# Performance work log

Measured on AMD Instinct MI355X. Metric: run time of the kernel, lower is better.

The kernel has to match this reference:

```python
import jax, jax.numpy as jnp
import numpy as np

DIM = 512
HEADS = 8
HEAD_DIM = DIM // HEADS

def setup_inputs() -> dict:
    key = jax.random.key(0)
    ks = jax.random.split(key, 5)
    s = 1.0 / np.sqrt(DIM)
    x = jax.random.normal(ks[0], (4, 2048, DIM), dtype=jnp.float32)
    w_qkv = jax.random.uniform(ks[1], (DIM, 3 * DIM), jnp.float32, -s, s)
    b_qkv = jax.random.uniform(ks[2], (3 * DIM,), jnp.float32, -s, s)
    w_out = jax.random.uniform(ks[3], (DIM, DIM), jnp.float32, -s, s)
    b_out = jax.random.uniform(ks[4], (DIM,), jnp.float32, -s, s)
    return {"x": x, "w_qkv": w_qkv, "b_qkv": b_qkv, "w_out": w_out, "b_out": b_out}

def reference(x, w_qkv, b_qkv, w_out, b_out):
    B, N, D = x.shape
    qkv = x @ w_qkv + b_qkv  # [B, N, 3D]
    qkv = qkv.reshape(B, N, 3, HEADS, HEAD_DIM).transpose(2, 0, 3, 1, 4)  # [3, B, H, N, hd]
    q, k, v = qkv[0], qkv[1], qkv[2]
    scale = 1.0 / np.sqrt(HEAD_DIM).astype(np.float32)
    attn = jnp.einsum('bhqd,bhkd->bhqk', q, k) * scale
    attn = jax.nn.softmax(attn, axis=-1)
    out = jnp.einsum('bhqk,bhkd->bhqd', attn, v)  # [B, H, N, hd]
    out = out.transpose(0, 2, 1, 3).reshape(B, N, D)
    return out @ w_out + b_out
```

## Files before the change

### kernel.cpp

```cpp
#include <hip/hip_runtime.h>

#define NB 4
#define NH 8
#define HD 64
#define DIMV 512
#define NSEQ 2048
#define QKVLD 1536
#define NTOK (NB*NSEQ)
#define KVB 64
#define QSCALE 0.18033688011112042f

typedef __attribute__((ext_vector_type(8))) short s8v;
typedef __attribute__((ext_vector_type(4))) float f4v;

typedef __attribute__((address_space(1))) void gvoid;
typedef __attribute__((address_space(3))) void lvoid;

__device__ __forceinline__ void load_lds16(const void* g, void* l){
  __builtin_amdgcn_global_load_lds((gvoid*)(void*)g, (lvoid*)l, 16, 0, 0);
}

__device__ __forceinline__ ushort f2bf(float f){
  unsigned u = __float_as_uint(f);
  u += 0x7fffu + ((u >> 16) & 1u);
  return (ushort)(u >> 16);
}

__device__ __forceinline__ unsigned pk2bf(float a, float b){
  return (unsigned)f2bf(a) | ((unsigned)f2bf(b) << 16);
}

__device__ __forceinline__ unsigned cvt_pk_bf16(float lo, float hi){
  unsigned r;
  asm("v_cvt_pk_bf16_f32 %0, %1, %2" : "=v"(r) : "v"(lo), "v"(hi));
  return r;
}
__device__ __forceinline__ float fexp2(float x){
  float r;
  asm("v_exp_f32 %0, %1" : "=v"(r) : "v"(x));
  return r;
}
__device__ __forceinline__ void plane32(unsigned &a, unsigned &b){
  asm("v_permlane32_swap_b32 %0, %1" : "+v"(a), "+v"(b));
}
__device__ __forceinline__ void plane16(unsigned &a, unsigned &b){
  asm("v_permlane16_swap_b32 %0, %1" : "+v"(a), "+v"(b));
}

__global__ __launch_bounds__(256) void k_prep(const float* __restrict__ x,
                                              ushort* __restrict__ xb,
                                              const float* __restrict__ w_qkv,
                                              ushort* __restrict__ wqkvT,
                                              const float* __restrict__ w_out,
                                              ushort* __restrict__ woutT){
  const int blk = blockIdx.x;
  const int tid = threadIdx.x;
  if (blk < 4096){
    const int i = blk * 256 + tid;
    float4 v = ((const float4*)x)[i];
    ushort4 o;
    o.x = f2bf(v.x); o.y = f2bf(v.y); o.z = f2bf(v.z); o.w = f2bf(v.w);
    ((ushort4*)xb)[i] = o;
    return;
  }
  __shared__ float t[32][33];
  const float* in; ushort* out; int C, bx, by;
  if (blk < 4864){
    const int idx = blk - 4096;
    in = w_qkv; out = wqkvT; C = QKVLD;
    bx = (idx % 48) * 32; by = (idx / 48) * 32;
  } else {
    const int idx = blk - 4864;
    in = w_out; out = woutT; C = DIMV;
    bx = (idx & 15) * 32; by = (idx >> 4) * 32;
  }
  const int tx = tid & 31, ty = tid >> 5;
  #pragma unroll
  for (int j = 0; j < 32; j += 8)
    t[ty + j][tx] = in[(size_t)(by + ty + j)*C + bx + tx];
  __syncthreads();
  #pragma unroll
  for (int j = 0; j < 32; j += 8)
    out[(size_t)(bx + ty + j)*DIMV + by + tx] = f2bf(t[tx][ty + j]);
}

template<bool SWAP>
__device__ __forceinline__ void gemm_kloop(const ushort* __restrict__ A,
                                           const ushort* __restrict__ Bt,
                                           ushort* As, ushort* Bs,
                                           int tm, int tn, int K,
                                           int w, int l, int lr, int lg,
                                           f4v acc[4][4]){
  const int r8 = l >> 3;
  const int lc = (l & 7) ^ r8;
  const int swz = (lr & 7) << 4;
  for (int kk = 0; kk < K; kk += 64){
    __syncthreads();
    #pragma unroll
    for (int c = 0; c < 4; ++c){
      const int ci = w*4 + c;
      const int row = ci*8 + r8;
      load_lds16(A  + (size_t)(tm + row)*K + kk + lc*8, (char*)As + ci*1024);
      load_lds16(Bt + (size_t)(tn + row)*K + kk + lc*8, (char*)Bs + ci*1024);
    }
    __syncthreads();
    const int wm = (w >> 1), wn = (w & 1);
    s8v af[4][2], bf[4][2];
    #pragma unroll
    for (int i = 0; i < 4; ++i){
      const int ra = (wm*64 + i*16 + lr)*128;
      const int rb = (wn*64 + i*16 + lr)*128;
      #pragma unroll
      for (int t = 0; t < 2; ++t){
        af[i][t] = *(const s8v*)((const char*)As + ra + ((t*64 + lg*16) ^ swz));
        bf[i][t] = *(const s8v*)((const char*)Bs + rb + ((t*64 + lg*16) ^ swz));
      }
    }
    #pragma unroll
    for (int mi = 0; mi < 4; ++mi)
      #pragma unroll
      for (int ni = 0; ni < 4; ++ni){
        if (SWAP){
          acc[mi][ni] = __builtin_amdgcn_mfma_f32_16x16x32_bf16(bf[ni][0], af[mi][0], acc[mi][ni], 0, 0, 0);
          acc[mi][ni] = __builtin_amdgcn_mfma_f32_16x16x32_bf16(bf[ni][1], af[mi][1], acc[mi][ni], 0, 0, 0);
        } else {
          acc[mi][ni] = __builtin_amdgcn_mfma_f32_16x16x32_bf16(af[mi][0], bf[ni][0], acc[mi][ni], 0, 0, 0);
          acc[mi][ni] = __builtin_amdgcn_mfma_f32_16x16x32_bf16(af[mi][1], bf[ni][1], acc[mi][ni], 0, 0, 0);
        }
      }
  }
}

template<int MODE, int NCT>
__global__ __launch_bounds__(256) void k_gemm(const ushort* __restrict__ A,
                                              const ushort* __restrict__ Bt,
                                              const float* __restrict__ bias,
                                              void* __restrict__ Cout,
                                              ushort* __restrict__ vtp,
                                              int N, int K){
  __shared__ ushort As[128*64];
  __shared__ ushort Bs[128*64];
  const int tid = threadIdx.x;
  const int w = tid >> 6, l = tid & 63;
  const int lr = l & 15, lg = l >> 4;
  const int wm = w >> 1, wn = w & 1;
  const int wg = blockIdx.x;
  const int xcd = wg & 7, idx = wg >> 3;
  const int tn = (idx % NCT) * 128;
  const int tm = (xcd * 8 + idx / NCT) * 128;
  f4v acc[4][4] = {};

  if (MODE == 0 && tn >= 2*DIMV){
    gemm_kloop<false>(A, Bt, As, Bs, tm, tn, K, w, l, lr, lg, acc);
    const int b = tm >> 11;
    const int n0 = (tm & (NSEQ-1)) + wm*64;
    #pragma unroll
    for (int ni = 0; ni < 4; ++ni){
      const int c = tn + wn*64 + ni*16 + lr;
      const int hd_i = c - 2*DIMV;
      const float bv = bias[c];
      ushort* vrow = vtp + ((size_t)(b*DIMV + hd_i))*NSEQ;
      #pragma unroll
      for (int mi = 0; mi < 4; ++mi){
        const int n = n0 + mi*16 + lg*4;
        uint2 pk;
        pk.x = pk2bf(acc[mi][ni][0] + bv, acc[mi][ni][1] + bv);
        pk.y = pk2bf(acc[mi][ni][2] + bv, acc[mi][ni][3] + bv);
        *(uint2*)(vrow + n) = pk;
      }
    }
    return;
  }

  gemm_kloop<true>(A, Bt, As, Bs, tm, tn, K, w, l, lr, lg, acc);

  if (MODE == 0){
    ushort* C = (ushort*)Cout;
    const float sc = (tn < DIMV) ? QSCALE : 1.0f;
    #pragma unroll
    for (int ni = 0; ni < 4; ++ni){
      const int c0 = tn + wn*64 + ni*16 + lg*4;
      const float4 bv = *(const float4*)(bias + c0);
      #pragma unroll
      for (int mi = 0; mi < 4; ++mi){
        const int r = tm + wm*64 + mi*16 + lr;
        uint2 pk;
        pk.x = pk2bf((acc[mi][ni][0] + bv.x)*sc, (acc[mi][ni][1] + bv.y)*sc);
        pk.y = pk2bf((acc[mi][ni][2] + bv.z)*sc, (acc[mi][ni][3] + bv.w)*sc);
        *(uint2*)(C + (size_t)r*N + c0) = pk;
      }
    }
  } else {
    float* C = (float*)Cout;
    #pragma unroll
    for (int ni = 0; ni < 4; ++ni){
      const int c0 = tn + wn*64 + ni*16 + lg*4;
      const float4 bv = *(const float4*)(bias + c0);
      #pragma unroll
      for (int mi = 0; mi < 4; ++mi){
        const int r = tm + wm*64 + mi*16 + lr;
        float4 st;
        st.x = acc[mi][ni][0] + bv.x;
        st.y = acc[mi][ni][1] + bv.y;
        st.z = acc[mi][ni][2] + bv.z;
        st.w = acc[mi][ni][3] + bv.w;
        *(float4*)(C + (size_t)r*N + c0) = st;
      }
    }
  }
}

__global__ __launch_bounds__(256, 2) void k_attn(const ushort* __restrict__ qkv,
                                                 const ushort* __restrict__ vt,
                                                 ushort* __restrict__ ao){
  __shared__ alignas(1024) char smem[2][16384];
  const int tid = threadIdx.x;
  const int w = tid >> 6, l = tid & 63;
  const int lr = l & 15, lg = l >> 4;
  const int wg = blockIdx.x;
  const int n = (wg & 7) * 64 + (wg >> 3);
  const int bh = n >> 4, xt = n & 15;
  const int b = bh >> 3, h = bh & 7;
  const int q0 = xt * 128 + w * 32;

  const ushort* qpA = qkv + (size_t)(b*NSEQ + q0 + lr)*QKVLD + h*HD + lg*8;
  const ushort* qpB = qpA + (size_t)16*QKVLD;
  const s8v qfA0 = *(const s8v*)(qpA);
  const s8v qfA1 = *(const s8v*)(qpA + 32);
  const s8v qfB0 = *(const s8v*)(qpB);
  const s8v qfB1 = *(const s8v*)(qpB + 32);

  const int r8 = l >> 3;
  const int lc = (l & 7) ^ r8;
  const int wbase = w * 16;
  const ushort* kg0 = qkv + (size_t)(b*NSEQ + wbase + r8)*QKVLD + DIMV + h*HD + lc*8;
  const ushort* kg1 = kg0 + (size_t)8*QKVLD;
  const ushort* vg0 = vt + (size_t)(bh*HD + wbase + r8)*NSEQ + lc*8;
  const ushort* vg1 = vg0 + (size_t)8*NSEQ;

  float lsumA = 0.0f, lsumB = 0.0f;
  f4v oA[4] = {}, oB[4] = {};

  load_lds16(kg0, &smem[0][ wbase   *128]);
  load_lds16(kg1, &smem[0][(wbase+8)*128]);
  load_lds16(vg0, &smem[0][ wbase   *128 + 8192]);
  load_lds16(vg1, &smem[0][(wbase+8)*128 + 8192]);
  kg0 += (size_t)KVB*QKVLD; kg1 += (size_t)KVB*QKVLD; vg0 += KVB; vg1 += KVB;

  const int swz = (lr & 7) << 4;
  const int ro0 = lr*128 + ((     lg*16) ^ swz);
  const int ro1 = lr*128 + ((64 + lg*16) ^ swz);

  for (int kt = 0; kt < NSEQ/KVB; ++kt){
    const int cur = kt & 1;
    __syncthreads();

    if (kt + 1 < NSEQ/KVB){
      char* dst = &smem[cur^1][0];
      load_lds16(kg0, dst +  wbase   *128);
      load_lds16(kg1, dst + (wbase+8)*128);
      load_lds16(vg0, dst +  wbase   *128 + 8192);
      load_lds16(vg1, dst + (wbase+8)*128 + 8192);
      kg0 += (size_t)KVB*QKVLD; kg1 += (size_t)KVB*QKVLD; vg0 += KVB; vg1 += KVB;
    }

    const char* b0 = &smem[cur][0] + ro0;
    const char* b1 = &smem[cur][0] + ro1;

    f4v sA[4] = {}, sB[4] = {};
    __builtin_amdgcn_s_setprio(1);
    #pragma unroll
    for (int kb = 0; kb < 4; ++kb){
      const s8v kf0 = *(const s8v*)(b0 + kb*2048);
      const s8v kf1 = *(const s8v*)(b1 + kb*2048);
      sA[kb] = __builtin_amdgcn_mfma_f32_16x16x32_bf16(kf0, qfA0, sA[kb], 0,0,0);
      sA[kb] = __builtin_amdgcn_mfma_f32_16x16x32_bf16(kf1, qfA1, sA[kb], 0,0,0);
      sB[kb] = __builtin_amdgcn_mfma_f32_16x16x32_bf16(kf0, qfB0, sB[kb], 0,0,0);
      sB[kb] = __builtin_amdgcn_mfma_f32_16x16x32_bf16(kf1, qfB1, sB[kb], 0,0,0);
    }
    __builtin_amdgcn_s_setprio(0);

    union { uint4 u; s8v v; } pfA0, pfA1, pfB0, pfB1;
    {
      const float p0 = fexp2(sA[0][0]), p1 = fexp2(sA[0][1]);
      const float p2 = fexp2(sA[0][2]), p3 = fexp2(sA[0][3]);
      const float p4 = fexp2(sA[1][0]), p5 = fexp2(sA[1][1]);
      const float p6 = fexp2(sA[1][2]), p7 = fexp2(sA[1][3]);
      lsumA += ((p0 + p1) + (p2 + p3)) + ((p4 + p5) + (p6 + p7));
      unsigned a = cvt_pk_bf16(p0, p1), bq = cvt_pk_bf16(p4, p5);
      plane32(a, bq); plane16(a, bq);
      unsigned c = cvt_pk_bf16(p2, p3), d = cvt_pk_bf16(p6, p7);
      plane32(c, d);  plane16(c, d);
      pfA0.u.x = a; pfA0.u.y = c; pfA0.u.z = bq; pfA0.u.w = d;
    }
    {
      const float p0 = fexp2(sA[2][0]), p1 = fexp2(sA[2][1]);
      const float p2 = fexp2(sA[2][2]), p3 = fexp2(sA[2][3]);
      const float p4 = fexp2(sA[3][0]), p5 = fexp2(sA[3][1]);
      const float p6 = fexp2(sA[3][2]), p7 = fexp2(sA[3][3]);
      lsumA += ((p0 + p1) + (p2 + p3)) + ((p4 + p5) + (p6 + p7));
      unsigned a = cvt_pk_bf16(p0, p1), bq = cvt_pk_bf16(p4, p5);
      plane32(a, bq); plane16(a, bq);
      unsigned c = cvt_pk_bf16(p2, p3), d = cvt_pk_bf16(p6, p7);
      plane32(c, d);  plane16(c, d);
      pfA1.u.x = a; pfA1.u.y = c; pfA1.u.z = bq; pfA1.u.w = d;
    }
    {
      const float p0 = fexp2(sB[0][0]), p1 = fexp2(sB[0][1]);
      const float p2 = fexp2(sB[0][2]), p3 = fexp2(sB[0][3]);
      const float p4 = fexp2(sB[1][0]), p5 = fexp2(sB[1][1]);
      const float p6 = fexp2(sB[1][2]), p7 = fexp2(sB[1][3]);
      lsumB += ((p0 + p1) + (p2 + p3)) + ((p4 + p5) + (p6 + p7));
      unsigned a = cvt_pk_bf16(p0, p1), bq = cvt_pk_bf16(p4, p5);
      plane32(a, bq); plane16(a, bq);
      unsigned c = cvt_pk_bf16(p2, p3), d = cvt_pk_bf16(p6, p7);
      plane32(c, d);  plane16(c, d);
      pfB0.u.x = a; pfB0.u.y = c; pfB0.u.z = bq; pfB0.u.w = d;
    }
    {
      const float p0 = fexp2(sB[2][0]), p1 = fexp2(sB[2][1]);
      const float p2 = fexp2(sB[2][2]), p3 = fexp2(sB[2][3]);
      const float p4 = fexp2(sB[3][0]), p5 = fexp2(sB[3][1]);
      const float p6 = fexp2(sB[3][2]), p7 = fexp2(sB[3][3]);
      lsumB += ((p0 + p1) + (p2 + p3)) + ((p4 + p5) + (p6 + p7));
      unsigned a = cvt_pk_bf16(p0, p1), bq = cvt_pk_bf16(p4, p5);
      plane32(a, bq); plane16(a, bq);
      unsigned c = cvt_pk_bf16(p2, p3), d = cvt_pk_bf16(p6, p7);
      plane32(c, d);  plane16(c, d);
      pfB1.u.x = a; pfB1.u.y = c; pfB1.u.z = bq; pfB1.u.w = d;
    }

    __builtin_amdgcn_s_setprio(1);
    #pragma unroll
    for (int ni = 0; ni < 4; ++ni){
      const s8v vf0 = *(const s8v*)(b0 + 8192 + ni*2048);
      const s8v vf1 = *(const s8v*)(b1 + 8192 + ni*2048);
      oA[ni] = __builtin_amdgcn_mfma_f32_16x16x32_bf16(vf0, pfA0.v, oA[ni], 0,0,0);
      oA[ni] = __builtin_amdgcn_mfma_f32_16x16x32_bf16(vf1, pfA1.v, oA[ni], 0,0,0);
      oB[ni] = __builtin_amdgcn_mfma_f32_16x16x32_bf16(vf0, pfB0.v, oB[ni], 0,0,0);
      oB[ni] = __builtin_amdgcn_mfma_f32_16x16x32_bf16(vf1, pfB1.v, oB[ni], 0,0,0);
    }
    __builtin_amdgcn_s_setprio(0);
  }

  float ltA = lsumA;
  ltA += __shfl_xor(ltA, 16, 64);
  ltA += __shfl_xor(ltA, 32, 64);
  float ltB = lsumB;
  ltB += __shfl_xor(ltB, 16, 64);
  ltB += __shfl_xor(ltB, 32, 64);
  const float invA = 1.0f / ltA;
  const float invB = 1.0f / ltB;
  ushort* opA = ao + (size_t)(b*NSEQ + q0 + lr)*DIMV + h*HD;
  ushort* opB = opA + (size_t)16*DIMV;
  #pragma unroll
  for (int ni = 0; ni < 4; ++ni){
    uint2 pk;
    pk.x = cvt_pk_bf16(oA[ni][0]*invA, oA[ni][1]*invA);
    pk.y = cvt_pk_bf16(oA[ni][2]*invA, oA[ni][3]*invA);
    *(uint2*)(opA + ni*16 + lg*4) = pk;
    pk.x = cvt_pk_bf16(oB[ni][0]*invB, oB[ni][1]*invB);
    pk.y = cvt_pk_bf16(oB[ni][2]*invB, oB[ni][3]*invB);
    *(uint2*)(opB + ni*16 + lg*4) = pk;
  }
}


extern "C" void kernel_launch(void* const* d_in, const int* in_sizes, int n_in,
                              void* d_out, int out_size, void* d_ws, size_t ws_size,
                              hipStream_t stream) {
  (void)in_sizes; (void)n_in; (void)out_size; (void)ws_size;
  const float* x     = (const float*)d_in[0];
  const float* w_qkv = (const float*)d_in[1];
  const float* b_qkv = (const float*)d_in[2];
  const float* w_out = (const float*)d_in[3];
  const float* b_out = (const float*)d_in[4];
  float* out = (float*)d_out;

  char* ws = (char*)d_ws;
  ushort* xb    = (ushort*)(ws);
  ushort* wqkvT = (ushort*)(ws + 8388608);
  ushort* woutT = (ushort*)(ws + 8388608 + 1572864);
  ushort* qkv   = (ushort*)(ws + 10485760);
  ushort* vt    = (ushort*)(ws + 35651584);
  ushort* ao    = (ushort*)(ws + 44040192);

  k_prep<<<dim3(4096 + 768 + 256), 256, 0, stream>>>(x, xb, w_qkv, wqkvT, w_out, woutT);
  k_gemm<0,12><<<dim3(768), 256, 0, stream>>>(xb, wqkvT, b_qkv, qkv, vt, QKVLD, DIMV);
  k_attn<<<dim3(512), 256, 0, stream>>>(qkv, vt, ao);
  k_gemm<1,4><<<dim3(256), 256, 0, stream>>>(ao, woutT, b_out, out, nullptr, DIMV, DIMV);
}
```

Measured before the change: 90.20 us.

## Fuse x fp32-to-bf16 conversion into QKV GEMM and compute softmax row sums via MFMA

Drops the separate conversion pass that wrote a bf16 copy of x. The QKV GEMM now loads fp32 x directly, converts it in registers and stores it into LDS, saving a 16 MB read plus an 8 MB write and round trip. The cost is that each x tile is re-converted by all 12 column tiles, and the A-operand path becomes synchronous register loads instead of async global-to-LDS. Separately, the attention kernel computes softmax denominators with an extra MFMA against a ones vector, removing scalar adds and cross-lane shuffles at the price of four more MFMAs per KV block and sums taken over bf16-rounded probabilities.

```diff
diff --git a/kernel.cpp b/kernel.cpp
--- a/kernel.cpp
+++ b/kernel.cpp
@@ -47,30 +47,19 @@
   asm("v_permlane16_swap_b32 %0, %1" : "+v"(a), "+v"(b));
 }
 
-__global__ __launch_bounds__(256) void k_prep(const float* __restrict__ x,
-                                              ushort* __restrict__ xb,
-                                              const float* __restrict__ w_qkv,
+__global__ __launch_bounds__(256) void k_prep(const float* __restrict__ w_qkv,
                                               ushort* __restrict__ wqkvT,
                                               const float* __restrict__ w_out,
                                               ushort* __restrict__ woutT){
   const int blk = blockIdx.x;
   const int tid = threadIdx.x;
-  if (blk < 4096){
-    const int i = blk * 256 + tid;
-    float4 v = ((const float4*)x)[i];
-    ushort4 o;
-    o.x = f2bf(v.x); o.y = f2bf(v.y); o.z = f2bf(v.z); o.w = f2bf(v.w);
-    ((ushort4*)xb)[i] = o;
-    return;
-  }
   __shared__ float t[32][33];
   const float* in; ushort* out; int C, bx, by;
-  if (blk < 4864){
-    const int idx = blk - 4096;
+  if (blk < 768){
     in = w_qkv; out = wqkvT; C = QKVLD;
-    bx = (idx % 48) * 32; by = (idx / 48) * 32;
+    bx = (blk % 48) * 32; by = (blk / 48) * 32;
   } else {
-    const int idx = blk - 4864;
+    const int idx = blk - 768;
     in = w_out; out = woutT; C = DIMV;
     bx = (idx & 15) * 32; by = (idx >> 4) * 32;
   }
@@ -84,8 +73,8 @@
     out[(size_t)(bx + ty + j)*DIMV + by + tx] = f2bf(t[tx][ty + j]);
 }
 
-template<bool SWAP>
-__device__ __forceinline__ void gemm_kloop(const ushort* __restrict__ A,
+template<bool SWAP, bool CONV>
+__device__ __forceinline__ void gemm_kloop(const void* __restrict__ Asrc,
                                            const ushort* __restrict__ Bt,
                                            ushort* As, ushort* Bs,
                                            int tm, int tn, int K,
@@ -100,7 +89,20 @@
     for (int c = 0; c < 4; ++c){
       const int ci = w*4 + c;
       const int row = ci*8 + r8;
-      load_lds16(A  + (size_t)(tm + row)*K + kk + lc*8, (char*)As + ci*1024);
+      if (CONV){
+        const float* xs = (const float*)Asrc + (size_t)(tm + row)*K + kk + lc*8;
+        const float4 a0 = *(const float4*)(xs);
+        const float4 a1 = *(const float4*)(xs + 4);
+        uint4 wb;
+        wb.x = cvt_pk_bf16(a0.x, a0.y);
+        wb.y = cvt_pk_bf16(a0.z, a0.w);
+        wb.z = cvt_pk_bf16(a1.x, a1.y);
+        wb.w = cvt_pk_bf16(a1.z, a1.w);
+        *(uint4*)((char*)As + ci*1024 + l*16) = wb;
+      } else {
+        load_lds16((const ushort*)Asrc + (size_t)(tm + row)*K + kk + lc*8,
+                   (char*)As + ci*1024);
+      }
       load_lds16(Bt + (size_t)(tn + row)*K + kk + lc*8, (char*)Bs + ci*1024);
     }
     __syncthreads();
@@ -132,7 +134,7 @@
 }
 
 template<int MODE, int NCT>
-__global__ __launch_bounds__(256) void k_gemm(const ushort* __restrict__ A,
+__global__ __launch_bounds__(256) void k_gemm(const void* __restrict__ A,
                                               const ushort* __restrict__ Bt,
                                               const float* __restrict__ bias,
                                               void* __restrict__ Cout,
@@ -151,7 +153,7 @@
   f4v acc[4][4] = {};
 
   if (MODE == 0 && tn >= 2*DIMV){
-    gemm_kloop<false>(A, Bt, As, Bs, tm, tn, K, w, l, lr, lg, acc);
+    gemm_kloop<false, true>(A, Bt, As, Bs, tm, tn, K, w, l, lr, lg, acc);
     const int b = tm >> 11;
     const int n0 = (tm & (NSEQ-1)) + wm*64;
     #pragma unroll
@@ -172,7 +174,8 @@
     return;
   }
 
-  gemm_kloop<true>(A, Bt, As, Bs, tm, tn, K, w, l, lr, lg, acc);
+  if (MODE == 0) gemm_kloop<true, true >(A, Bt, As, Bs, tm, tn, K, w, l, lr, lg, acc);
+  else           gemm_kloop<true, false>(A, Bt, As, Bs, tm, tn, K, w, l, lr, lg, acc);
 
   if (MODE == 0){
     ushort* C = (ushort*)Cout;
@@ -230,6 +233,10 @@
   const s8v qfB0 = *(const s8v*)(qpB);
   const s8v qfB1 = *(const s8v*)(qpB + 32);
 
+  union { uint4 u; s8v v; } ones;
+  ones.u.x = 0x3F803F80u; ones.u.y = 0x3F803F80u;
+  ones.u.z = 0x3F803F80u; ones.u.w = 0x3F803F80u;
+
   const int r8 = l >> 3;
   const int lc = (l & 7) ^ r8;
   const int wbase = w * 16;
@@ -238,7 +245,7 @@
   const ushort* vg0 = vt + (size_t)(bh*HD + wbase + r8)*NSEQ + lc*8;
   const ushort* vg1 = vg0 + (size_t)8*NSEQ;
 
-  float lsumA = 0.0f, lsumB = 0.0f;
+  f4v lsA = {}, lsB = {};
   f4v oA[4] = {}, oB[4] = {};
 
   load_lds16(kg0, &smem[0][ wbase   *128]);
@@ -286,7 +293,6 @@
       const float p2 = fexp2(sA[0][2]), p3 = fexp2(sA[0][3]);
       const float p4 = fexp2(sA[1][0]), p5 = fexp2(sA[1][1]);
       const float p6 = fexp2(sA[1][2]), p7 = fexp2(sA[1][3]);
-      lsumA += ((p0 + p1) + (p2 + p3)) + ((p4 + p5) + (p6 + p7));
       unsigned a = cvt_pk_bf16(p0, p1), bq = cvt_pk_bf16(p4, p5);
       plane32(a, bq); plane16(a, bq);
       unsigned c = cvt_pk_bf16(p2, p3), d = cvt_pk_bf16(p6, p7);
@@ -298,7 +304,6 @@
       const float p2 = fexp2(sA[2][2]), p3 = fexp2(sA[2][3]);
       const float p4 = fexp2(sA[3][0]), p5 = fexp2(sA[3][1]);
       const float p6 = fexp2(sA[3][2]), p7 = fexp2(sA[3][3]);
-      lsumA += ((p0 + p1) + (p2 + p3)) + ((p4 + p5) + (p6 + p7));
       unsigned a = cvt_pk_bf16(p0, p1), bq = cvt_pk_bf16(p4, p5);
       plane32(a, bq); plane16(a, bq);
       unsigned c = cvt_pk_bf16(p2, p3), d = cvt_pk_bf16(p6, p7);
@@ -310,7 +315,6 @@
       const float p2 = fexp2(sB[0][2]), p3 = fexp2(sB[0][3]);
       const float p4 = fexp2(sB[1][0]), p5 = fexp2(sB[1][1]);
       const float p6 = fexp2(sB[1][2]), p7 = fexp2(sB[1][3]);
-      lsumB += ((p0 + p1) + (p2 + p3)) + ((p4 + p5) + (p6 + p7));
       unsigned a = cvt_pk_bf16(p0, p1), bq = cvt_pk_bf16(p4, p5);
       plane32(a, bq); plane16(a, bq);
       unsigned c = cvt_pk_bf16(p2, p3), d = cvt_pk_bf16(p6, p7);
@@ -322,7 +326,6 @@
       const float p2 = fexp2(sB[2][2]), p3 = fexp2(sB[2][3]);
       const float p4 = fexp2(sB[3][0]), p5 = fexp2(sB[3][1]);
       const float p6 = fexp2(sB[3][2]), p7 = fexp2(sB[3][3]);
-      lsumB += ((p0 + p1) + (p2 + p3)) + ((p4 + p5) + (p6 + p7));
       unsigned a = cvt_pk_bf16(p0, p1), bq = cvt_pk_bf16(p4, p5);
       plane32(a, bq); plane16(a, bq);
       unsigned c = cvt_pk_bf16(p2, p3), d = cvt_pk_bf16(p6, p7);
@@ -340,17 +343,15 @@
       oB[ni] = __builtin_amdgcn_mfma_f32_16x16x32_bf16(vf0, pfB0.v, oB[ni], 0,0,0);
       oB[ni] = __builtin_amdgcn_mfma_f32_16x16x32_bf16(vf1, pfB1.v, oB[ni], 0,0,0);
     }
+    lsA = __builtin_amdgcn_mfma_f32_16x16x32_bf16(ones.v, pfA0.v, lsA, 0,0,0);
+    lsA = __builtin_amdgcn_mfma_f32_16x16x32_bf16(ones.v, pfA1.v, lsA, 0,0,0);
+    lsB = __builtin_amdgcn_mfma_f32_16x16x32_bf16(ones.v, pfB0.v, lsB, 0,0,0);
+    lsB = __builtin_amdgcn_mfma_f32_16x16x32_bf16(ones.v, pfB1.v, lsB, 0,0,0);
     __builtin_amdgcn_s_setprio(0);
   }
 
-  float ltA = lsumA;
-  ltA += __shfl_xor(ltA, 16, 64);
-  ltA += __shfl_xor(ltA, 32, 64);
-  float ltB = lsumB;
-  ltB += __shfl_xor(ltB, 16, 64);
-  ltB += __shfl_xor(ltB, 32, 64);
-  const float invA = 1.0f / ltA;
-  const float invB = 1.0f / ltB;
+  const float invA = 1.0f / lsA[0];
+  const float invB = 1.0f / lsB[0];
   ushort* opA = ao + (size_t)(b*NSEQ + q0 + lr)*DIMV + h*HD;
   ushort* opB = opA + (size_t)16*DIMV;
   #pragma unroll
@@ -378,15 +379,14 @@
   float* out = (float*)d_out;
 
   char* ws = (char*)d_ws;
-  ushort* xb    = (ushort*)(ws);
   ushort* wqkvT = (ushort*)(ws + 8388608);
   ushort* woutT = (ushort*)(ws + 8388608 + 1572864);
   ushort* qkv   = (ushort*)(ws + 10485760);
   ushort* vt    = (ushort*)(ws + 35651584);
   ushort* ao    = (ushort*)(ws + 44040192);
 
-  k_prep<<<dim3(4096 + 768 + 256), 256, 0, stream>>>(x, xb, w_qkv, wqkvT, w_out, woutT);
-  k_gemm<0,12><<<dim3(768), 256, 0, stream>>>(xb, wqkvT, b_qkv, qkv, vt, QKVLD, DIMV);
+  k_prep<<<dim3(1024), 256, 0, stream>>>(w_qkv, wqkvT, w_out, woutT);
+  k_gemm<0,12><<<dim3(768), 256, 0, stream>>>(x, wqkvT, b_qkv, qkv, vt, QKVLD, DIMV);
   k_attn<<<dim3(512), 256, 0, stream>>>(qkv, vt, ao);
   k_gemm<1,4><<<dim3(256), 256, 0, stream>>>(ao, woutT, b_out, out, nullptr, DIMV, DIMV);
 }
```

Measured after the change: 94.34 us. 4.6% more time.

## Double-buffer GEMM K-loop with 32-wide slices and narrower output-projection tiles

Applied to the files above, without the earlier changes.

Rewrites the GEMM main loop to use BK=32 tiles held in two LDS buffers. The next slice is prefetched via global_load_lds while the current one feeds MFMA, which removes one barrier per iteration and overlaps loads with compute. The output projection gets its own kernel with 128x64 tiles, launched as 512 blocks instead of 256, to fill more CUs. In exchange, each slice does less MFMA work per barrier and the kernel carries a new swizzle layout.

```diff
diff --git a/kernel.cpp b/kernel.cpp
--- a/kernel.cpp
+++ b/kernel.cpp
@@ -85,61 +85,68 @@
 }
 
 template<bool SWAP>
-__device__ __forceinline__ void gemm_kloop(const ushort* __restrict__ A,
-                                           const ushort* __restrict__ Bt,
-                                           ushort* As, ushort* Bs,
-                                           int tm, int tn, int K,
-                                           int w, int l, int lr, int lg,
-                                           f4v acc[4][4]){
-  const int r8 = l >> 3;
-  const int lc = (l & 7) ^ r8;
-  const int swz = (lr & 7) << 4;
-  for (int kk = 0; kk < K; kk += 64){
+__device__ __forceinline__ void gemm_kloop32(const ushort* __restrict__ A,
+                                             const ushort* __restrict__ Bt,
+                                             ushort (*As)[128*32], ushort (*Bs)[128*32],
+                                             int tm, int tn, int K,
+                                             int w, int l, int lr, int lg,
+                                             f4v acc[4][4]){
+  const int r16 = l >> 2;
+  const int lc  = (l & 3) ^ ((l >> 3) & 3);
+  const int wm = w >> 1, wn = w & 1;
+  const ushort* ag0 = A  + (size_t)(tm + 32*w + r16)*K + lc*8;
+  const ushort* ag1 = ag0 + (size_t)16*K;
+  const ushort* bg0 = Bt + (size_t)(tn + 32*w + r16)*K + lc*8;
+  const ushort* bg1 = bg0 + (size_t)16*K;
+
+  load_lds16(ag0, (char*)As[0] + (2*w  )*1024);
+  load_lds16(ag1, (char*)As[0] + (2*w+1)*1024);
+  load_lds16(bg0, (char*)Bs[0] + (2*w  )*1024);
+  load_lds16(bg1, (char*)Bs[0] + (2*w+1)*1024);
+  ag0 += 32; ag1 += 32; bg0 += 32; bg1 += 32;
+
+  const int rosw = ((lr >> 1) & 3) << 4;
+  const int roA = (wm*64 + lr)*64 + ((lg*16) ^ rosw);
+  const int roB = (wn*64 + lr)*64 + ((lg*16) ^ rosw);
+
+  const int NIT = K >> 5;
+  for (int kt = 0; kt < NIT; ++kt){
+    const int cur = kt & 1;
     __syncthreads();
-    #pragma unroll
-    for (int c = 0; c < 4; ++c){
-      const int ci = w*4 + c;
-      const int row = ci*8 + r8;
-      load_lds16(A  + (size_t)(tm + row)*K + kk + lc*8, (char*)As + ci*1024);
-      load_lds16(Bt + (size_t)(tn + row)*K + kk + lc*8, (char*)Bs + ci*1024);
-    }
-    __syncthreads();
-    const int wm = (w >> 1), wn = (w & 1);
-    s8v af[4][2], bf[4][2];
+    if (kt + 1 < NIT){
+      load_lds16(ag0, (char*)As[cur^1] + (2*w  )*1024);
+      load_lds16(ag1, (char*)As[cur^1] + (2*w+1)*1024);
+      load_lds16(bg0, (char*)Bs[cur^1] + (2*w  )*1024);
+      load_lds16(bg1, (char*)Bs[cur^1] + (2*w+1)*1024);
+      ag0 += 32; ag1 += 32; bg0 += 32; bg1 += 32;
+    }
+    s8v af[4], bf[4];
     #pragma unroll
     for (int i = 0; i < 4; ++i){
-      const int ra = (wm*64 + i*16 + lr)*128;
-      const int rb = (wn*64 + i*16 + lr)*128;
-      #pragma unroll
-      for (int t = 0; t < 2; ++t){
-        af[i][t] = *(const s8v*)((const char*)As + ra + ((t*64 + lg*16) ^ swz));
-        bf[i][t] = *(const s8v*)((const char*)Bs + rb + ((t*64 + lg*16) ^ swz));
-      }
+      af[i] = *(const s8v*)((const char*)As[cur] + roA + i*1024);
+      bf[i] = *(const s8v*)((const char*)Bs[cur] + roB + i*1024);
     }
     #pragma unroll
     for (int mi = 0; mi < 4; ++mi)
       #pragma unroll
       for (int ni = 0; ni < 4; ++ni){
-        if (SWAP){
-          acc[mi][ni] = __builtin_amdgcn_mfma_f32_16x16x32_bf16(bf[ni][0], af[mi][0], acc[mi][ni], 0, 0, 0);
-          acc[mi][ni] = __builtin_amdgcn_mfma_f32_16x16x32_bf16(bf[ni][1], af[mi][1], acc[mi][ni], 0, 0, 0);
-        } else {
-          acc[mi][ni] = __builtin_amdgcn_mfma_f32_16x16x32_bf16(af[mi][0], bf[ni][0], acc[mi][ni], 0, 0, 0);
-          acc[mi][ni] = __builtin_amdgcn_mfma_f32_16x16x32_bf16(af[mi][1], bf[ni][1], acc[mi][ni], 0, 0, 0);
-        }
+        if (SWAP)
+          acc[mi][ni] = __builtin_amdgcn_mfma_f32_16x16x32_bf16(bf[ni], af[mi], acc[mi][ni], 0, 0, 0);
+        else
+          acc[mi][ni] = __builtin_amdgcn_mfma_f32_16x16x32_bf16(af[mi], bf[ni], acc[mi][ni], 0, 0, 0);
       }
   }
 }
 
-template<int MODE, int NCT>
+template<int NCT>
 __global__ __launch_bounds__(256) void k_gemm(const ushort* __restrict__ A,
                                               const ushort* __restrict__ Bt,
                                               const float* __restrict__ bias,
                                               void* __restrict__ Cout,
                                               ushort* __restrict__ vtp,
                                               int N, int K){
-  __shared__ ushort As[128*64];
-  __shared__ ushort Bs[128*64];
+  __shared__ ushort As[2][128*32];
+  __shared__ ushort Bs[2][128*32];
   const int tid = threadIdx.x;
   const int w = tid >> 6, l = tid & 63;
   const int lr = l & 15, lg = l >> 4;
@@ -150,8 +157,8 @@
   const int tm = (xcd * 8 + idx / NCT) * 128;
   f4v acc[4][4] = {};
 
-  if (MODE == 0 && tn >= 2*DIMV){
-    gemm_kloop<false>(A, Bt, As, Bs, tm, tn, K, w, l, lr, lg, acc);
+  if (tn >= 2*DIMV){
+    gemm_kloop32<false>(A, Bt, As, Bs, tm, tn, K, w, l, lr, lg, acc);
     const int b = tm >> 11;
     const int n0 = (tm & (NSEQ-1)) + wm*64;
     #pragma unroll
@@ -172,40 +179,93 @@
     return;
   }
 
-  gemm_kloop<true>(A, Bt, As, Bs, tm, tn, K, w, l, lr, lg, acc);
-
-  if (MODE == 0){
-    ushort* C = (ushort*)Cout;
-    const float sc = (tn < DIMV) ? QSCALE : 1.0f;
-    #pragma unroll
-    for (int ni = 0; ni < 4; ++ni){
-      const int c0 = tn + wn*64 + ni*16 + lg*4;
-      const float4 bv = *(const float4*)(bias + c0);
+  gemm_kloop32<true>(A, Bt, As, Bs, tm, tn, K, w, l, lr, lg, acc);
+
+  ushort* C = (ushort*)Cout;
+  const float sc = (tn < DIMV) ? QSCALE : 1.0f;
+  #pragma unroll
+  for (int ni = 0; ni < 4; ++ni){
+    const int c0 = tn + wn*64 + ni*16 + lg*4;
+    const float4 bv = *(const float4*)(bias + c0);
+    #pragma unroll
+    for (int mi = 0; mi < 4; ++mi){
+      const int r = tm + wm*64 + mi*16 + lr;
+      uint2 pk;
+      pk.x = pk2bf((acc[mi][ni][0] + bv.x)*sc, (acc[mi][ni][1] + bv.y)*sc);
+      pk.y = pk2bf((acc[mi][ni][2] + bv.z)*sc, (acc[mi][ni][3] + bv.w)*sc);
+      *(uint2*)(C + (size_t)r*N + c0) = pk;
+    }
+  }
+}
+
+__global__ __launch_bounds__(256) void k_gemm2(const ushort* __restrict__ A,
+                                               const ushort* __restrict__ Bt,
+                                               const float* __restrict__ bias,
+                                               float* __restrict__ Cout){
+  __shared__ ushort As[2][128*32];
+  __shared__ ushort Bs[2][64*32];
+  const int tid = threadIdx.x;
+  const int w = tid >> 6, l = tid & 63;
+  const int lr = l & 15, lg = l >> 4;
+  const int wm = w >> 1, wn = w & 1;
+  const int wg = blockIdx.x;
+  const int xcd = wg & 7, idx = wg >> 3;
+  const int tn = (idx & 7) * 64;
+  const int tm = (xcd * 8 + (idx >> 3)) * 128;
+  const int K = DIMV;
+  const int r16 = l >> 2;
+  const int lc  = (l & 3) ^ ((l >> 3) & 3);
+  f4v acc[4][2] = {};
+
+  const ushort* ag0 = A  + (size_t)(tm + 32*w + r16)*K + lc*8;
+  const ushort* ag1 = ag0 + (size_t)16*K;
+  const ushort* bg0 = Bt + (size_t)(tn + 16*w + r16)*K + lc*8;
+
+  load_lds16(ag0, (char*)As[0] + (2*w  )*1024);
+  load_lds16(ag1, (char*)As[0] + (2*w+1)*1024);
+  load_lds16(bg0, (char*)Bs[0] + w*1024);
+  ag0 += 32; ag1 += 32; bg0 += 32;
+
+  const int rosw = ((lr >> 1) & 3) << 4;
+  const int roA = (wm*64 + lr)*64 + ((lg*16) ^ rosw);
+  const int roB = (wn*32 + lr)*64 + ((lg*16) ^ rosw);
+
+  for (int kt = 0; kt < K/32; ++kt){
+    const int cur = kt & 1;
+    __syncthreads();
+    if (kt + 1 < K/32){
+      load_lds16(ag0, (char*)As[cur^1] + (2*w  )*1024);
+      load_lds16(ag1, (char*)As[cur^1] + (2*w+1)*1024);
+      load_lds16(bg0, (char*)Bs[cur^1] + w*1024);
+      ag0 += 32; ag1 += 32; bg0 += 32;
+    }
+    s8v af[4], bf[2];
+    #pragma unroll
+    for (int i = 0; i < 4; ++i)
+      af[i] = *(const s8v*)((const char*)As[cur] + roA + i*1024);
+    #pragma unroll
+    for (int i = 0; i < 2; ++i)
+      bf[i] = *(const s8v*)((const char*)Bs[cur] + roB + i*1024);
+    #pragma unroll
+    for (int mi = 0; mi < 4; ++mi)
       #pragma unroll
-      for (int mi = 0; mi < 4; ++mi){
-        const int r = tm + wm*64 + mi*16 + lr;
-        uint2 pk;
-        pk.x = pk2bf((acc[mi][ni][0] + bv.x)*sc, (acc[mi][ni][1] + bv.y)*sc);
-        pk.y = pk2bf((acc[mi][ni][2] + bv.z)*sc, (acc[mi][ni][3] + bv.w)*sc);
-        *(uint2*)(C + (size_t)r*N + c0) = pk;
-      }
-    }
-  } else {
-    float* C = (float*)Cout;
-    #pragma unroll
-    for (int ni = 0; ni < 4; ++ni){
-      const int c0 = tn + wn*64 + ni*16 + lg*4;
-      const float4 bv = *(const float4*)(bias + c0);
-      #pragma unroll
-      for (int mi = 0; mi < 4; ++mi){
-        const int r = tm + wm*64 + mi*16 + lr;
-        float4 st;
-        st.x = acc[mi][ni][0] + bv.x;
-        st.y = acc[mi][ni][1] + bv.y;
-        st.z = acc[mi][ni][2] + bv.z;
-        st.w = acc[mi][ni][3] + bv.w;
-        *(float4*)(C + (size_t)r*N + c0) = st;
-      }
+      for (int ni = 0; ni < 2; ++ni)
+        acc[mi][ni] = __builtin_amdgcn_mfma_f32_16x16x32_bf16(bf[ni], af[mi], acc[mi][ni], 0, 0, 0);
+  }
+
+  #pragma unroll
+  for (int ni = 0; ni < 2; ++ni){
+    const int c0 = tn + wn*32 + ni*16 + lg*4;
+    const float4 bv = *(const float4*)(bias + c0);
+    #pragma unroll
+    for (int mi = 0; mi < 4; ++mi){
+      const int r = tm + wm*64 + mi*16 + lr;
+      float4 st;
+      st.x = acc[mi][ni][0] + bv.x;
+      st.y = acc[mi][ni][1] + bv.y;
+      st.z = acc[mi][ni][2] + bv.z;
+      st.w = acc[mi][ni][3] + bv.w;
+      *(float4*)(Cout + (size_t)r*DIMV + c0) = st;
     }
   }
 }
@@ -386,7 +446,7 @@
   ushort* ao    = (ushort*)(ws + 44040192);
 
   k_prep<<<dim3(4096 + 768 + 256), 256, 0, stream>>>(x, xb, w_qkv, wqkvT, w_out, woutT);
-  k_gemm<0,12><<<dim3(768), 256, 0, stream>>>(xb, wqkvT, b_qkv, qkv, vt, QKVLD, DIMV);
+  k_gemm<12><<<dim3(768), 256, 0, stream>>>(xb, wqkvT, b_qkv, qkv, vt, QKVLD, DIMV);
   k_attn<<<dim3(512), 256, 0, stream>>>(qkv, vt, ao);
-  k_gemm<1,4><<<dim3(256), 256, 0, stream>>>(ao, woutT, b_out, out, nullptr, DIMV, DIMV);
-}
+  k_gemm2<<<dim3(512), 256, 0, stream>>>(ao, woutT, b_out, out);
+}
```

Measured after the change: 90.07 us. About the same (-0.1%).
